# Optimization experiments

Hardware: AMD Instinct MI355X
Metric: run time of the kernel (lower is better)

## Reference

```python
import jax, jax.numpy as jnp
import numpy as np

N_NODES = 16384
K_NBR = 16
N_HOPS = 4  # hops + 2
IN_DIM = 256
RAW_DIM = 128
OUT_DIM = 64
PHI_DIM = 16
N_KERN = 4
E = N_NODES * K_NBR


def setup_inputs() -> dict:
    key = jax.random.key(0)
    ks = jax.random.split(key, 16)
    s = 0.05  # small weight scale for numerical sanity
    h = jax.random.normal(ks[0], (N_NODES, IN_DIM), jnp.float32)
    e_tensor = jax.random.normal(ks[1], (N_HOPS, N_NODES, RAW_DIM), jnp.float32)
    # kNN-style edges: each dst node has exactly K_NBR incoming edges
    src = jax.random.randint(ks[2], (N_HOPS, E), 0, N_NODES, jnp.int32)
    dst = jnp.tile(jnp.repeat(jnp.arange(N_NODES, dtype=jnp.int32), K_NBR)[None, :], (N_HOPS, 1))
    return {
        'h': h,
        'e_tensor': e_tensor,
        'src': src,
        'dst': dst,
        'W_phi': jax.random.normal(ks[3], (N_HOPS, RAW_DIM, PHI_DIM - 1), jnp.float32) * s,
        'mlp_w1': jax.random.normal(ks[4], (N_HOPS, RAW_DIM, IN_DIM), jnp.float32) * s,
        'mlp_b1': jax.random.normal(ks[5], (N_HOPS, IN_DIM), jnp.float32) * s,
        'mlp_w2': jax.random.normal(ks[6], (N_HOPS, IN_DIM, PHI_DIM * N_KERN), jnp.float32) * s,
        'mlp_b2': jax.random.normal(ks[7], (N_HOPS, PHI_DIM * N_KERN), jnp.float32) * s,
        'tilde_phi': jax.random.normal(ks[8], (N_HOPS, N_KERN, PHI_DIM), jnp.float32),
        'W': jax.random.normal(ks[9], (N_HOPS, IN_DIM, OUT_DIM * N_KERN), jnp.float32) * s,
        'bias': jax.random.normal(ks[10], (N_HOPS, OUT_DIM), jnp.float32) * s,
        'z': jax.random.normal(ks[11], (OUT_DIM, 1), jnp.float32),
    }


def _deform_gconv(h, e_l, src, dst, W_phi, w1, b1, w2, b2, tilde_phi, W, bias):
    N = h.shape[0]
    nk, phi_dim = tilde_phi.shape
    hk = (h @ W).reshape(N, nk, -1)                                  # (N, nk, out)
    phi = e_l @ W_phi                                                # (N, phi-1)
    tn = tilde_phi / jnp.linalg.norm(tilde_phi, axis=1, keepdims=True)  # (nk, phi)
    hid = jax.nn.relu(e_l @ w1 + b1)
    delta = (hid @ w2 + b2).reshape(N, nk, phi_dim)                  # (N, nk, phi)
    delta_ik = tn[None, :, :] + delta                                # (N, nk, phi)
    # per-edge quantities (edges carry dst-node delta_ik, u_sub_v distance)
    dist = phi[src] - phi[dst]                                       # (E, phi-1)
    last = jnp.all(dist == 0, axis=1, keepdims=True).astype(dist.dtype)
    dist = jnp.concatenate([dist, last], axis=1)                     # (E, phi)
    dist = dist / jnp.maximum(jnp.linalg.norm(dist, axis=1, keepdims=True), 1e-8)
    logits = jnp.einsum('ep,ekp->ek', dist, delta_ik[dst])           # (E, nk)
    # edge_softmax over incoming edges of each dst node
    mx = jax.ops.segment_max(logits, dst, num_segments=N)
    ex = jnp.exp(logits - mx[dst])
    den = jax.ops.segment_sum(ex, dst, num_segments=N)
    att = ex / den[dst]                                              # (E, nk)
    # message passing: m = h[src] * att, sum over incoming edges
    m = hk[src] * att[:, :, None]                                    # (E, nk, out)
    agg = jax.ops.segment_sum(m, dst, num_segments=N)                # (N, nk, out)
    out = agg.sum(1) + bias[None, :]
    out = out / jnp.maximum(jnp.linalg.norm(out, axis=1, keepdims=True), 1e-8)
    # regularizers
    d = tn[:, None, :] - tn[None, :, :]                              # (nk, nk, phi)
    l_sep = jnp.sum(jnp.sum(d * d, axis=-1)) / nk                    # sum_i mean_j ||t_i - t_j||^2
    l_focus = jnp.mean(jnp.sum(delta * delta, axis=2))
    return out, l_sep, l_focus


def reference(h, e_tensor, src, dst, W_phi, mlp_w1, mlp_b1, mlp_w2, mlp_b2, tilde_phi, W, bias, z):
    outs, l_seps, l_fos = jax.vmap(
        _deform_gconv, in_axes=(None, 0, 0, 0, 0, 0, 0, 0, 0, 0, 0, 0)
    )(h, e_tensor, src, dst, W_phi, mlp_w1, mlp_b1, mlp_w2, mlp_b2, tilde_phi, W, bias)
    # hop-level softmax fusion
    score = jnp.einsum('hno,oz->hnz', outs, z)                       # (n_hops, N, 1)
    att = jax.nn.softmax(score, axis=0)
    tilde_h = jnp.sum(att * outs, axis=0)                            # (N, out)
    l_sep = jnp.mean(l_seps)
    l_focus = jnp.mean(l_fos)
    return tilde_h, l_sep, l_focus
```

## Files before the change

kernel.cpp:

```cpp
#include <hip/hip_runtime.h>
#include <hip/hip_bf16.h>

#define N_NODES 16384
#define K_NBR 16
#define HOPS 4
#define IN_DIM 256
#define RAW_DIM 128
#define OUT_DIM 64
#define PHI_DIM 16
#define N_KERN 4
#define E_EDGES (N_NODES * K_NBR)

typedef __hip_bfloat16 bf16;
typedef __attribute__((ext_vector_type(8))) short short8;
typedef __attribute__((ext_vector_type(4))) float f32x4;
typedef __attribute__((ext_vector_type(2))) float f32x2;
typedef __attribute__((ext_vector_type(4))) unsigned int uint4v;

__device__ __forceinline__ float toF(float x) { return x; }
__device__ __forceinline__ float toF(bf16 x) { return __bfloat162float(x); }
__device__ __forceinline__ short f2bfbits(float f)
{
    bf16 b = __float2bfloat16(f);
    short s; __builtin_memcpy(&s, &b, 2); return s;
}

#define SWZ(row, colShort) ((colShort) ^ (((row) & 7) << 3))
#define SWZ32(row, colShort) ((colShort) ^ ((((row) >> 1) & 3) << 3))

__device__ __forceinline__ void gld_lds16(const bf16* g, short* l)
{
    __builtin_amdgcn_global_load_lds(
        (const __attribute__((address_space(1))) unsigned int*)g,
        (__attribute__((address_space(3))) unsigned int*)l, 16, 0, 0);
}

template <int IMM>
__device__ __forceinline__ float swzx(float v)
{
    return __builtin_bit_cast(float,
        __builtin_amdgcn_ds_swizzle(__builtin_bit_cast(int, v), IMM));
}
#define XOR1  0x041F
#define XOR2  0x081F
#define XOR4  0x101F
#define XOR8  0x201F
#define XOR16 0x401F

__device__ __forceinline__ void pkfma_w0(f32x2& acc, f32x2 w, f32x2 x)
{
    asm("v_pk_fma_f32 %0, %1, %2, %0 op_sel:[0,0,0] op_sel_hi:[0,1,1]"
        : "+v"(acc) : "v"(w), "v"(x));
}
__device__ __forceinline__ void pkfma_w1(f32x2& acc, f32x2 w, f32x2 x)
{
    asm("v_pk_fma_f32 %0, %1, %2, %0 op_sel:[1,0,0] op_sel_hi:[1,1,1]"
        : "+v"(acc) : "v"(w), "v"(x));
}

#define CV_WPHI 0
#define CV_W1   (CV_WPHI + HOPS * RAW_DIM * (PHI_DIM - 1))
#define CV_B1   (CV_W1 + HOPS * RAW_DIM * IN_DIM)
#define CV_W2   (CV_B1 + HOPS * IN_DIM)
#define CV_B2   (CV_W2 + HOPS * IN_DIM * PHI_DIM * N_KERN)
#define CV_TPHI (CV_B2 + HOPS * PHI_DIM * N_KERN)
#define CV_W    (CV_TPHI + HOPS * N_KERN * PHI_DIM)
#define CV_BIAS (CV_W + HOPS * IN_DIM * OUT_DIM * N_KERN)
#define CV_Z    (CV_BIAS + HOPS * OUT_DIM)
#define CV_END  (CV_Z + OUT_DIM)

#define WT_N  (HOPS * 256 * 256)
#define W1T_N (HOPS * 256 * 128)
#define W2T_N (HOPS * 64 * 256)
#define WPT_N (HOPS * 16 * 128)
#define CVT_TOTAL (WT_N + W1T_N + W2T_N + WPT_N)

#define NB_CV ((CV_END + 255) / 256)
#define NB_WT (CVT_TOTAL / 256)
#define NB_H  (N_NODES * 256 / 8 / 256)
#define NB_E  (HOPS * N_NODES * 128 / 8 / 256)
#define NB_ALL (NB_CV + NB_WT + NB_H + NB_E + 1)

#define GA_TOTAL 2048

__device__ __forceinline__ float loadDyn(const void* p, int i, bool isbf)
{
    return isbf ? toF(((const bf16*)p)[i]) : ((const float*)p)[i];
}

__device__ __forceinline__ void cvt8(bf16* dst, const void* src, size_t base, bool isbf)
{
    short8 v;
    if (isbf) {
        v = *(const short8*)((const bf16*)src + base);
    } else {
        const float* sp = (const float*)src + base;
        f32x4 f0 = *(const f32x4*)sp;
        f32x4 f1 = *(const f32x4*)(sp + 4);
#pragma unroll
        for (int j = 0; j < 4; j++) { v[j] = f2bfbits(f0[j]); v[4 + j] = f2bfbits(f1[j]); }
    }
    *(short8*)(dst + base) = v;
}

__global__ __launch_bounds__(256) void cvt_all(
    const void* h, const void* e,
    const void* wphi, const void* w1, const void* b1, const void* w2,
    const void* b2, const void* tphi, const void* W, const void* bias,
    const void* z, float* __restrict__ CV,
    bf16* __restrict__ wt, bf16* __restrict__ w1t, bf16* __restrict__ w2t,
    bf16* __restrict__ wpt, bf16* __restrict__ h_bf, bf16* __restrict__ e_bf,
    float* __restrict__ tn_out, float* __restrict__ acc, int* __restrict__ flagOut)
{
    __shared__ float s_det[4];
    int tid = threadIdx.x;
    {
        unsigned short pv = ((const unsigned short*)h)[tid];
        unsigned int bits = ((unsigned int)pv) << 16;
        float v; __builtin_memcpy(&v, &bits, 4);
        v = fabsf(v);
        if (!(v == v) || v > 1e30f) v = 1e30f;
#pragma unroll
        for (int off = 32; off > 0; off >>= 1) v = fmaxf(v, __shfl_xor(v, off));
        if ((tid & 63) == 0) s_det[tid >> 6] = v;
    }
    __syncthreads();
    bool isbf = fmaxf(fmaxf(s_det[0], s_det[1]), fmaxf(s_det[2], s_det[3])) < 1e4f;

    int b = blockIdx.x;
    if (b == NB_ALL - 1) {
        __shared__ float s_v[256], s_tn[256], s_red[256], s_hop[4];
        int hop = tid >> 6, t64 = tid & 63;
        int row = t64 >> 4, p = t64 & 15;
        float v = loadDyn(tphi, hop * 64 + t64, isbf);
        s_v[tid] = v;
        __syncthreads();
        float ss = 0.f;
        for (int q = 0; q < 16; q++) { float x = s_v[hop * 64 + row * 16 + q]; ss += x * x; }
        float tnv = v / sqrtf(ss);
        tn_out[hop * 64 + t64] = tnv;
        s_tn[tid] = tnv;
        __syncthreads();
        float s = 0.f;
        for (int j = 0; j < 4; j++) {
            float d = tnv - s_tn[hop * 64 + j * 16 + p];
            s += d * d;
        }
        s_red[tid] = s;
        __syncthreads();
        if (t64 == 0) {
            float tot = 0.f;
            for (int i = 0; i < 64; i++) tot += s_red[hop * 64 + i];
            s_hop[hop] = tot;
        }
        __syncthreads();
        if (tid == 0) {
            acc[0] = (s_hop[0] + s_hop[1] + s_hop[2] + s_hop[3]) * 0.0625f;
            acc[1] = 0.f;
            *flagOut = isbf ? 1 : 0;
        }
        return;
    }
    if (b < NB_CV) {
        int idx = b * 256 + tid;
        if (idx >= CV_END) return;
        float v;
        if      (idx < CV_W1)   v = loadDyn(wphi, idx - CV_WPHI, isbf);
        else if (idx < CV_B1)   v = loadDyn(w1,   idx - CV_W1,   isbf);
        else if (idx < CV_W2)   v = loadDyn(b1,   idx - CV_B1,   isbf);
        else if (idx < CV_B2)   v = loadDyn(w2,   idx - CV_W2,   isbf);
        else if (idx < CV_TPHI) v = loadDyn(b2,   idx - CV_B2,   isbf);
        else if (idx < CV_W)    v = loadDyn(tphi, idx - CV_TPHI, isbf);
        else if (idx < CV_BIAS) v = loadDyn(W,    idx - CV_W,    isbf);
        else if (idx < CV_Z)    v = loadDyn(bias, idx - CV_BIAS, isbf);
        else                    v = loadDyn(z,    idx - CV_Z,    isbf);
        CV[idx] = v;
        return;
    }
    b -= NB_CV;
    if (b < NB_WT) {
        int idx = b * 256 + tid;
        if (idx < WT_N) {
            int o = idx, hop = o >> 16, rem = o & 65535, n = rem >> 8, k = rem & 255;
            wt[o] = __float2bfloat16(loadDyn(W, hop * 65536 + k * 256 + n, isbf));
        } else if (idx < WT_N + W1T_N) {
            int o = idx - WT_N, hop = o >> 15, rem = o & 32767, n = rem >> 7, k = rem & 127;
            w1t[o] = __float2bfloat16(loadDyn(w1, hop * 32768 + k * 256 + n, isbf));
        } else if (idx < WT_N + W1T_N + W2T_N) {
            int o = idx - WT_N - W1T_N, hop = o >> 14, rem = o & 16383, n = rem >> 8, k = rem & 255;
            w2t[o] = __float2bfloat16(loadDyn(w2, hop * 16384 + k * 64 + n, isbf));
        } else {
            int o = idx - WT_N - W1T_N - W2T_N, hop = o >> 11, rem = o & 2047, n = rem >> 7, k = rem & 127;
            float v = (n < 15) ? loadDyn(wphi, hop * 1920 + k * 15 + n, isbf) : 0.f;
            wpt[o] = __float2bfloat16(v);
        }
        return;
    }
    b -= NB_WT;
    if (b < NB_H) {
        size_t base = ((size_t)b * 256 + tid) * 8;
        cvt8(h_bf, h, base, isbf);
        return;
    }
    b -= NB_H;
    {
        size_t base = ((size_t)b * 256 + tid) * 8;
        cvt8(e_bf, e, base, isbf);
    }
}

__device__ __forceinline__ void gemm_hk_dev(
    char* smem, const bf16* __restrict__ A, const bf16* __restrict__ Bt,
    unsigned char* __restrict__ Cg, int colBase, int rowBase)
{
    short* base = (short*)smem;
    int tid = threadIdx.x;
    int w = tid >> 6, lane = tid & 63;
    int wr = w >> 1, wc = w & 1;
    int l16 = lane & 15, quad = lane >> 4;
    f32x4 acc[4][4] = {};

#define HK_STAGE(bufb, k0v)                                                          \
    {                                                                                \
        short* As_ = base + (bufb) * 8192;                                           \
        short* Bs_ = As_ + 4096;                                                     \
        for (int id = tid; id < 128 * 4; id += 256) {                                \
            int row = id >> 2, j = id & 3;                                           \
            gld_lds16(A + (size_t)(rowBase + row) * 256 + (k0v) +                    \
                          ((j ^ ((row >> 1) & 3)) * 8),                              \
                      As_ + id * 8);                                                 \
        }                                                                            \
        for (int id = tid; id < 128 * 4; id += 256) {                                \
            int row = id >> 2, j = id & 3;                                           \
            gld_lds16(Bt + (size_t)(colBase + row) * 256 + (k0v) +                   \
                          ((j ^ ((row >> 1) & 3)) * 8),                              \
                      Bs_ + id * 8);                                                 \
        }                                                                            \
    }

    HK_STAGE(0, 0)
    __syncthreads();
    for (int t = 0; t < 8; ++t) {
        if (t < 7) HK_STAGE((t + 1) & 1, (t + 1) * 32)
        short* As = base + (t & 1) * 8192;
        short* Bs = As + 4096;
        short8 aF[4], bF[4];
#pragma unroll
        for (int mi = 0; mi < 4; mi++) {
            int row = wr * 64 + mi * 16 + l16;
            aF[mi] = *(const short8*)&As[row * 32 + SWZ32(row, quad * 8)];
        }
#pragma unroll
        for (int ni = 0; ni < 4; ni++) {
            int row = wc * 64 + ni * 16 + l16;
            bF[ni] = *(const short8*)&Bs[row * 32 + SWZ32(row, quad * 8)];
        }
#pragma unroll
        for (int mi = 0; mi < 4; mi++)
#pragma unroll
            for (int ni = 0; ni < 4; ni++)
                acc[mi][ni] = __builtin_amdgcn_mfma_f32_16x16x32_bf16(
                    aF[mi], bF[ni], acc[mi][ni], 0, 0, 0);
        __syncthreads();
    }
#undef HK_STAGE

    unsigned char* Cs = (unsigned char*)smem;
#pragma unroll
    for (int mi = 0; mi < 4; mi++)
#pragma unroll
        for (int ni = 0; ni < 4; ni++) {
            int cl = wc * 64 + ni * 16 + l16;
#pragma unroll
            for (int r = 0; r < 4; r++) {
                int rl = wr * 64 + mi * 16 + quad * 4 + r;
                float v = acc[mi][ni][r];
                int pk = __builtin_amdgcn_cvt_pk_fp8_f32(v, v, 0, false);
                Cs[rl * 128 + cl] = (unsigned char)(pk & 0xFF);
            }
        }
    __syncthreads();
    for (int c = tid; c < 128 * 8; c += 256) {
        int r = c >> 3, off = (c & 7) * 16;
        *(uint4v*)(Cg + ((size_t)(rowBase + r) * 256 + colBase) + off) =
            *(const uint4v*)(Cs + (size_t)r * 128 + off);
    }
}

__device__ __forceinline__ void hid_delta_dev(
    char* smem,
    const bf16* __restrict__ A, const bf16* __restrict__ B1,
    const bf16* __restrict__ B2, const bf16* __restrict__ WP,
    const float* __restrict__ b1, const float* __restrict__ b2,
    const float* __restrict__ tn, float* __restrict__ Dg,
    float* __restrict__ phiG, float* __restrict__ lfocus, int rowBase)
{
    short* As  = (short*)smem;
    short* Bs  = As + 64 * 64;
    short* Wpa = As + 20480;
    short* Hs  = (short*)smem;
    short* B2s = Hs + 64 * 256;
    float* Ds  = (float*)smem;
    float* s_w = (float*)(smem + 40944);

    int tid = threadIdx.x;
    int w = tid >> 6, lane = tid & 63;
    int l16 = lane & 15, quad = lane >> 4;

    {
        f32x4 acc[4][4] = {};
        f32x4 accp[4] = {};
        for (int k0 = 0; k0 < 128; k0 += 64) {
            for (int id = tid; id < 64 * 8; id += 256) {
                int row = id >> 3, j = id & 7;
                gld_lds16(A + (size_t)(rowBase + row) * 128 + k0 + ((j ^ (row & 7)) * 8),
                          As + id * 8);
            }
            for (int id = tid; id < 256 * 8; id += 256) {
                int row = id >> 3, j = id & 7;
                gld_lds16(B1 + (size_t)row * 128 + k0 + ((j ^ (row & 7)) * 8),
                          Bs + id * 8);
            }
            if (k0 == 0) {
                int row = tid >> 4, j = tid & 15;
                gld_lds16(WP + (size_t)row * 128 + ((j ^ (row & 7)) * 8),
                          Wpa + tid * 8);
            }
            __syncthreads();
#pragma unroll
            for (int kc = 0; kc < 64; kc += 32) {
                short8 aF[4], bF[4];
#pragma unroll
                for (int mi = 0; mi < 4; mi++) {
                    int row = mi * 16 + l16;
                    aF[mi] = *(const short8*)&As[row * 64 + SWZ(row, kc + quad * 8)];
                }
#pragma unroll
                for (int ni = 0; ni < 4; ni++) {
                    int row = w * 64 + ni * 16 + l16;
                    bF[ni] = *(const short8*)&Bs[row * 64 + SWZ(row, kc + quad * 8)];
                }
#pragma unroll
                for (int mi = 0; mi < 4; mi++)
#pragma unroll
                    for (int ni = 0; ni < 4; ni++)
                        acc[mi][ni] = __builtin_amdgcn_mfma_f32_16x16x32_bf16(
                            aF[mi], bF[ni], acc[mi][ni], 0, 0, 0);
                if (w == 0) {
                    short8 bFp = *(const short8*)&Wpa[l16 * 128 + SWZ(l16, k0 + kc + quad * 8)];
#pragma unroll
                    for (int mi = 0; mi < 4; mi++)
                        accp[mi] = __builtin_amdgcn_mfma_f32_16x16x32_bf16(
                            aF[mi], bFp, accp[mi], 0, 0, 0);
                }
            }
            __syncthreads();
        }
#pragma unroll
        for (int mi = 0; mi < 4; mi++) {
#pragma unroll
            for (int ni = 0; ni < 4; ni++) {
                int col = w * 64 + ni * 16 + l16;
                float bv = b1[col];
#pragma unroll
                for (int r = 0; r < 4; r++) {
                    int row = mi * 16 + quad * 4 + r;
                    float v = fmaxf(acc[mi][ni][r] + bv, 0.f);
                    Hs[row * 256 + SWZ(row, col)] = f2bfbits(v);
                }
            }
        }
        for (int id = tid; id < 64 * 8; id += 256) {
            int row = id >> 3, j = id & 7;
            gld_lds16(B2 + (size_t)row * 256 + ((j ^ (row & 7)) * 8),
                      B2s + id * 8);
        }
        if (w == 0) {
#pragma unroll
            for (int mi = 0; mi < 4; mi++)
#pragma unroll
                for (int r = 0; r < 4; r++)
                    phiG[(size_t)(rowBase + mi * 16 + quad * 4 + r) * 16 + l16] =
                        accp[mi][r];
        }
    }

    {
        f32x4 acc2[4] = {};
        for (int q = 0; q < 4; q++) {
            __syncthreads();
#pragma unroll
            for (int kcq = 0; kcq < 64; kcq += 32) {
                int arow = w * 16 + l16;
                short8 aF = *(const short8*)&Hs[arow * 256 + SWZ(arow, q * 64 + kcq + quad * 8)];
                short8 bF[4];
#pragma unroll
                for (int ni = 0; ni < 4; ni++) {
                    int row = ni * 16 + l16;
                    bF[ni] = *(const short8*)&B2s[row * 64 + SWZ(row, kcq + quad * 8)];
                }
#pragma unroll
                for (int ni = 0; ni < 4; ni++)
                    acc2[ni] = __builtin_amdgcn_mfma_f32_16x16x32_bf16(aF, bF[ni], acc2[ni], 0, 0, 0);
            }
            if (q < 3) {
                __syncthreads();
                for (int id = tid; id < 64 * 8; id += 256) {
                    int row = id >> 3, j = id & 7;
                    gld_lds16(B2 + (size_t)row * 256 + (q + 1) * 64 + ((j ^ (row & 7)) * 8),
                              B2s + id * 8);
                }
            }
        }
        __syncthreads();
        float sq = 0.f;
#pragma unroll
        for (int ni = 0; ni < 4; ni++) {
            int col = ni * 16 + l16;
            float bv = b2[col], tv = tn[col];
#pragma unroll
            for (int r = 0; r < 4; r++) {
                int row = w * 16 + quad * 4 + r;
                float v = acc2[ni][r] + bv;
                sq += v * v;
                Ds[row * 64 + col] = v + tv;
            }
        }
#pragma unroll
        for (int off = 32; off > 0; off >>= 1) sq += __shfl_xor(sq, off);
        if (lane == 0) s_w[w] = sq;
        __syncthreads();
        for (int c = tid; c < 64 * 16; c += 256) {
            int r = c >> 4, off = (c & 15) * 4;
            *(uint4v*)(Dg + (size_t)(rowBase + r) * 64 + off) =
                *(const uint4v*)(Ds + (size_t)r * 64 + off);
        }
        if (tid == 0) atomicAdd(lfocus, s_w[0] + s_w[1] + s_w[2] + s_w[3]);
    }
}

__global__ __launch_bounds__(256) void gemm_all(
    const bf16* __restrict__ h_bf, const bf16* __restrict__ e_bf,
    const bf16* __restrict__ WT, const bf16* __restrict__ WPT,
    const bf16* __restrict__ W1T, const bf16* __restrict__ W2T,
    const float* __restrict__ b1All, const float* __restrict__ b2All,
    const float* __restrict__ tnAll, unsigned char* __restrict__ hk_f8,
    float* __restrict__ phi, float* __restrict__ DELTA, float* __restrict__ lfocus)
{
    __shared__ __align__(16) char smem[45056];
    int b = blockIdx.x;
    bool isA = ((b >> 3) & 1) == 0;
    int a = ((b >> 4) << 3) | (b & 7);
    int hop = a >> 8;
    if (isA) {
        int r = a & 255, part = r >> 7, row = r & 127;
        gemm_hk_dev(smem, h_bf, WT + (size_t)hop * 65536,
                    hk_f8 + (size_t)hop * N_NODES * 256, part * 128, row * 128);
    } else {
        int tile = a & 255;
        hid_delta_dev(smem,
            e_bf + (size_t)hop * N_NODES * 128,
            W1T + (size_t)hop * 32768, W2T + (size_t)hop * 16384,
            WPT + (size_t)hop * 2048,
            b1All + hop * 256, b2All + hop * 64, tnAll + hop * 64,
            DELTA + (size_t)hop * N_NODES * 64,
            phi + (size_t)hop * N_NODES * 16, lfocus, tile * 64);
    }
}

__global__ __launch_bounds__(256) void edge_agg2(
    const unsigned char* __restrict__ hk, const float* __restrict__ phi,
    const float* __restrict__ dik, const int* __restrict__ src,
    const float* __restrict__ biasAll, float* __restrict__ outs)
{
    int b = blockIdx.x;
    int hop = b & 3;
    int wave = threadIdx.x >> 6, lane = threadIdx.x & 63;
    int node = (b >> 2) * 4 + wave;
    const unsigned char* hk_l = hk + (size_t)hop * N_NODES * 256;
    const float* phi_l  = phi + (size_t)hop * N_NODES * 16;
    const float* dik_l  = dik + (size_t)hop * N_NODES * 64;
    const int*   src_n  = src + (size_t)hop * E_EDGES + (size_t)node * 16;
    const float* bias_l = biasAll + hop * 64;
    float*       outs_n = outs + ((size_t)hop * N_NODES + node) * 64;

    __shared__ __align__(16) float s_dik[4][64];
    __shared__ __align__(16) float s_attT[4][4][24];
    __shared__ int   s_src[4][16];

    s_dik[wave][lane] = dik_l[(size_t)node * 64 + lane];
    if (lane < 16) s_src[wave][lane] = src_n[lane];

    int e = lane >> 2, q = lane & 3;
    int sN = s_src[wave][e];
    f32x4 ps = *(const f32x4*)(phi_l + (size_t)sN * 16 + q * 4);
    f32x4 pd = *(const f32x4*)(phi_l + (size_t)node * 16 + q * 4);
    float d0 = ps[0] - pd[0], d1 = ps[1] - pd[1];
    float d2 = ps[2] - pd[2], d3 = ps[3] - pd[3];
    bool q3 = (q == 3);
    float ssp = d0 * d0 + d1 * d1 + d2 * d2 + (q3 ? 0.f : d3 * d3);
    ssp += swzx<XOR1>(ssp); ssp += swzx<XOR2>(ssp);
    float last = (ssp == 0.f) ? 1.f : 0.f;
    if (q3) d3 = last;
    float inv = fminf(__builtin_amdgcn_rsqf(ssp + last * last), 1e8f);
#pragma unroll
    for (int k = 0; k < 4; k++) {
        f32x4 dkv = *(const f32x4*)&s_dik[wave][k * 16 + q * 4];
        float pk = d0 * dkv[0] + d1 * dkv[1] + d2 * dkv[2] + d3 * dkv[3];
        pk += swzx<XOR1>(pk); pk += swzx<XOR2>(pk);
        if (q == k) s_attT[wave][k][e] = pk * inv;
    }

    int k2 = lane & 3;
    float lgv = s_attT[wave][k2][e];
    float mx = lgv;
    mx = fmaxf(mx, swzx<XOR4>(mx));
    mx = fmaxf(mx, swzx<XOR8>(mx));
    mx = fmaxf(mx, swzx<XOR16>(mx));
    mx = fmaxf(mx, __shfl_xor(mx, 32));
    float ex = __expf(lgv - mx);
    float den = ex;
    den += swzx<XOR4>(den);
    den += swzx<XOR8>(den);
    den += swzx<XOR16>(den);
    den += __shfl_xor(den, 32);
    s_attT[wave][k2][e] = ex * __builtin_amdgcn_rcpf(den);

    int kk = lane >> 4, dsub = (lane & 15) * 4;
    f32x2 att2[8];
#pragma unroll
    for (int g = 0; g < 8; g++) att2[g] = *(const f32x2*)&s_attT[wave][kk][g * 2];
    f32x2 a01 = {0.f, 0.f}, a23 = {0.f, 0.f};
#pragma unroll
    for (int ep = 0; ep < 8; ep++) {
        int sm0 = __builtin_amdgcn_readfirstlane(s_src[wave][2 * ep]);
        int sm1 = __builtin_amdgcn_readfirstlane(s_src[wave][2 * ep + 1]);
        unsigned int u0 = *(const unsigned int*)(hk_l + (size_t)sm0 * 256 + lane * 4);
        unsigned int u1 = *(const unsigned int*)(hk_l + (size_t)sm1 * 256 + lane * 4);
        f32x2 w = att2[ep];
        pkfma_w0(a01, w, __builtin_amdgcn_cvt_pk_f32_fp8((int)u0, false));
        pkfma_w0(a23, w, __builtin_amdgcn_cvt_pk_f32_fp8((int)u0, true));
        pkfma_w1(a01, w, __builtin_amdgcn_cvt_pk_f32_fp8((int)u1, false));
        pkfma_w1(a23, w, __builtin_amdgcn_cvt_pk_f32_fp8((int)u1, true));
    }
    float a0 = a01[0], a1 = a01[1], a2 = a23[0], a3 = a23[1];
    a0 += swzx<XOR16>(a0); a0 += __shfl_xor(a0, 32);
    a1 += swzx<XOR16>(a1); a1 += __shfl_xor(a1, 32);
    a2 += swzx<XOR16>(a2); a2 += __shfl_xor(a2, 32);
    a3 += swzx<XOR16>(a3); a3 += __shfl_xor(a3, 32);
    f32x4 bv = *(const f32x4*)(bias_l + dsub);
    float o0 = a0 + bv[0];
    float o1 = a1 + bv[1];
    float o2 = a2 + bv[2];
    float o3 = a3 + bv[3];
    float ssq = o0 * o0 + o1 * o1 + o2 * o2 + o3 * o3;
    ssq += swzx<XOR1>(ssq);
    ssq += swzx<XOR2>(ssq);
    ssq += swzx<XOR4>(ssq);
    ssq += swzx<XOR8>(ssq);
    float inv2 = fminf(__builtin_amdgcn_rsqf(ssq), 1e8f);
    if (kk == 0) {
        f32x4 st;
        st[0] = o0 * inv2; st[1] = o1 * inv2; st[2] = o2 * inv2; st[3] = o3 * inv2;
        *(f32x4*)(outs_n + dsub) = st;
    }
}

__global__ __launch_bounds__(256) void fuse_kernel(
    const float* __restrict__ outs, const float* __restrict__ z,
    void* __restrict__ out, const int* __restrict__ flag,
    const float* __restrict__ acc)
{
    int tid = threadIdx.x;
    int node = blockIdx.x * 4 + (tid >> 6);
    int dd = tid & 63;
    float zv = z[dd];
    float o[4], sc[4];
#pragma unroll
    for (int h = 0; h < 4; h++) {
        o[h] = outs[((size_t)h * N_NODES + node) * 64 + dd];
        float v = o[h] * zv;
#pragma unroll
        for (int off = 32; off > 0; off >>= 1) v += __shfl_xor(v, off);
        sc[h] = v;
    }
    float mx = fmaxf(fmaxf(sc[0], sc[1]), fmaxf(sc[2], sc[3]));
    float e0 = __expf(sc[0] - mx), e1 = __expf(sc[1] - mx);
    float e2 = __expf(sc[2] - mx), e3 = __expf(sc[3] - mx);
    float den = e0 + e1 + e2 + e3;
    float t = (e0 * o[0] + e1 * o[1] + e2 * o[2] + e3 * o[3]) * __builtin_amdgcn_rcpf(den);
    size_t oi = (size_t)node * 64 + dd;
    bool isbf = (*flag != 0);
    if (isbf) ((bf16*)out)[oi] = __float2bfloat16(t);
    else      ((float*)out)[oi] = t;
    if (blockIdx.x == 0 && tid == 0) {
        float a = acc[0];
        float b = acc[1] / ((float)N_NODES * 4.f * 4.f);
        size_t base = (size_t)N_NODES * 64;
        if (isbf) {
            ((bf16*)out)[base]     = __float2bfloat16(a);
            ((bf16*)out)[base + 1] = __float2bfloat16(b);
        } else {
            ((float*)out)[base]     = a;
            ((float*)out)[base + 1] = b;
        }
    }
}

extern "C" void kernel_launch(void* const* d_in, const int* in_sizes, int n_in,
                              void* d_out, int out_size, void* d_ws, size_t ws_size,
                              hipStream_t stream)
{
    const void* h    = d_in[0];
    const void* e    = d_in[1];
    const int*  src  = (const int*)d_in[2];
    const void* Wphi = d_in[4];
    const void* w1   = d_in[5];
    const void* b1   = d_in[6];
    const void* w2   = d_in[7];
    const void* b2   = d_in[8];
    const void* tphi = d_in[9];
    const void* W    = d_in[10];
    const void* bias = d_in[11];
    const void* z    = d_in[12];

    float* ws    = (float*)d_ws;
    float* CV    = ws;
    float* OUTS  = CV + CV_END;
    float* PHI   = OUTS + (size_t)4 * N_NODES * 64;
    float* DELTA = PHI + (size_t)4 * N_NODES * 16;
    float* TN    = DELTA + (size_t)4 * N_NODES * 64;
    float* ACC   = TN + 256;
    int*   FLAG  = (int*)(ACC + 2);
    bf16*  H_BF  = (bf16*)(ACC + 4);
    bf16*  E_BF  = H_BF + (size_t)N_NODES * 256;
    bf16*  WT    = E_BF + (size_t)HOPS * N_NODES * 128;
    bf16*  W1T   = WT + WT_N;
    bf16*  W2T   = W1T + W1T_N;
    bf16*  WPT   = W2T + W2T_N;
    unsigned char* HK_F8 = (unsigned char*)(WPT + WPT_N);

    cvt_all<<<NB_ALL, 256, 0, stream>>>(
        h, e, Wphi, w1, b1, w2, b2, tphi, W, bias, z, CV,
        WT, W1T, W2T, WPT, H_BF, E_BF, TN, ACC, FLAG);

    gemm_all<<<dim3(GA_TOTAL), 256, 0, stream>>>(
        H_BF, E_BF, WT, WPT, W1T, W2T,
        CV + CV_B1, CV + CV_B2, TN, HK_F8, PHI, DELTA, ACC + 1);

    edge_agg2<<<dim3(N_NODES), 256, 0, stream>>>(
        HK_F8, PHI, DELTA, src, CV + CV_BIAS, OUTS);

    fuse_kernel<<<dim3(N_NODES / 4), 256, 0, stream>>>(
        OUTS, CV + CV_Z, d_out, FLAG, ACC);
}
```

Measured before the change: 200.5 us.

## Compact constant copy, coarsen conversion blocks, remap GEMM block order

The constant buffer now holds only the biases and z vector, no longer the full weight matrices, which the GEMMs read from transposed bf16 copies anyway. The conversion kernel processes more elements per thread (4 weight elements, 8 vector chunks), cutting block count. The GEMM block index mapping is reordered so that the eight blocks sharing a row-group span hop and column halves, which is meant to improve L2 reuse of the h rows across concurrently running blocks.

```diff
diff --git a/kernel.cpp b/kernel.cpp
--- a/kernel.cpp
+++ b/kernel.cpp
@@ -58,16 +58,11 @@
         : "+v"(acc) : "v"(w), "v"(x));
 }
 
-#define CV_WPHI 0
-#define CV_W1   (CV_WPHI + HOPS * RAW_DIM * (PHI_DIM - 1))
-#define CV_B1   (CV_W1 + HOPS * RAW_DIM * IN_DIM)
-#define CV_W2   (CV_B1 + HOPS * IN_DIM)
-#define CV_B2   (CV_W2 + HOPS * IN_DIM * PHI_DIM * N_KERN)
-#define CV_TPHI (CV_B2 + HOPS * PHI_DIM * N_KERN)
-#define CV_W    (CV_TPHI + HOPS * N_KERN * PHI_DIM)
-#define CV_BIAS (CV_W + HOPS * IN_DIM * OUT_DIM * N_KERN)
-#define CV_Z    (CV_BIAS + HOPS * OUT_DIM)
-#define CV_END  (CV_Z + OUT_DIM)
+#define CVC_B1   0
+#define CVC_B2   (CVC_B1 + HOPS * IN_DIM)
+#define CVC_BIAS (CVC_B2 + HOPS * PHI_DIM * N_KERN)
+#define CVC_Z    (CVC_BIAS + HOPS * OUT_DIM)
+#define CVC_END  (CVC_Z + OUT_DIM)
 
 #define WT_N  (HOPS * 256 * 256)
 #define W1T_N (HOPS * 256 * 128)
@@ -75,10 +70,10 @@
 #define WPT_N (HOPS * 16 * 128)
 #define CVT_TOTAL (WT_N + W1T_N + W2T_N + WPT_N)
 
-#define NB_CV ((CV_END + 255) / 256)
-#define NB_WT (CVT_TOTAL / 256)
-#define NB_H  (N_NODES * 256 / 8 / 256)
-#define NB_E  (HOPS * N_NODES * 128 / 8 / 256)
+#define NB_CV ((CVC_END + 255) / 256)
+#define NB_WT (CVT_TOTAL / 1024)
+#define NB_H  (N_NODES * 256 / 8 / 2048)
+#define NB_E  (HOPS * N_NODES * 128 / 8 / 2048)
 #define NB_ALL (NB_CV + NB_WT + NB_H + NB_E + 1)
 
 #define GA_TOTAL 2048
@@ -163,49 +158,54 @@
     }
     if (b < NB_CV) {
         int idx = b * 256 + tid;
-        if (idx >= CV_END) return;
+        if (idx >= CVC_END) return;
         float v;
-        if      (idx < CV_W1)   v = loadDyn(wphi, idx - CV_WPHI, isbf);
-        else if (idx < CV_B1)   v = loadDyn(w1,   idx - CV_W1,   isbf);
-        else if (idx < CV_W2)   v = loadDyn(b1,   idx - CV_B1,   isbf);
-        else if (idx < CV_B2)   v = loadDyn(w2,   idx - CV_W2,   isbf);
-        else if (idx < CV_TPHI) v = loadDyn(b2,   idx - CV_B2,   isbf);
-        else if (idx < CV_W)    v = loadDyn(tphi, idx - CV_TPHI, isbf);
-        else if (idx < CV_BIAS) v = loadDyn(W,    idx - CV_W,    isbf);
-        else if (idx < CV_Z)    v = loadDyn(bias, idx - CV_BIAS, isbf);
-        else                    v = loadDyn(z,    idx - CV_Z,    isbf);
+        if      (idx < CVC_B2)   v = loadDyn(b1,   idx - CVC_B1,   isbf);
+        else if (idx < CVC_BIAS) v = loadDyn(b2,   idx - CVC_B2,   isbf);
+        else if (idx < CVC_Z)    v = loadDyn(bias, idx - CVC_BIAS, isbf);
+        else                     v = loadDyn(z,    idx - CVC_Z,    isbf);
         CV[idx] = v;
         return;
     }
     b -= NB_CV;
     if (b < NB_WT) {
-        int idx = b * 256 + tid;
-        if (idx < WT_N) {
-            int o = idx, hop = o >> 16, rem = o & 65535, n = rem >> 8, k = rem & 255;
-            wt[o] = __float2bfloat16(loadDyn(W, hop * 65536 + k * 256 + n, isbf));
-        } else if (idx < WT_N + W1T_N) {
-            int o = idx - WT_N, hop = o >> 15, rem = o & 32767, n = rem >> 7, k = rem & 127;
-            w1t[o] = __float2bfloat16(loadDyn(w1, hop * 32768 + k * 256 + n, isbf));
-        } else if (idx < WT_N + W1T_N + W2T_N) {
-            int o = idx - WT_N - W1T_N, hop = o >> 14, rem = o & 16383, n = rem >> 8, k = rem & 255;
-            w2t[o] = __float2bfloat16(loadDyn(w2, hop * 16384 + k * 64 + n, isbf));
-        } else {
-            int o = idx - WT_N - W1T_N - W2T_N, hop = o >> 11, rem = o & 2047, n = rem >> 7, k = rem & 127;
-            float v = (n < 15) ? loadDyn(wphi, hop * 1920 + k * 15 + n, isbf) : 0.f;
-            wpt[o] = __float2bfloat16(v);
+        int base = (b * 256 + tid) * 4;
+#pragma unroll
+        for (int jj = 0; jj < 4; jj++) {
+            int idx = base + jj;
+            if (idx < WT_N) {
+                int o = idx, hop = o >> 16, rem = o & 65535, n = rem >> 8, k = rem & 255;
+                wt[o] = __float2bfloat16(loadDyn(W, hop * 65536 + k * 256 + n, isbf));
+            } else if (idx < WT_N + W1T_N) {
+                int o = idx - WT_N, hop = o >> 15, rem = o & 32767, n = rem >> 7, k = rem & 127;
+                w1t[o] = __float2bfloat16(loadDyn(w1, hop * 32768 + k * 256 + n, isbf));
+            } else if (idx < WT_N + W1T_N + W2T_N) {
+                int o = idx - WT_N - W1T_N, hop = o >> 14, rem = o & 16383, n = rem >> 8, k = rem & 255;
+                w2t[o] = __float2bfloat16(loadDyn(w2, hop * 16384 + k * 64 + n, isbf));
+            } else {
+                int o = idx - WT_N - W1T_N - W2T_N, hop = o >> 11, rem = o & 2047, n = rem >> 7, k = rem & 127;
+                float v = (n < 15) ? loadDyn(wphi, hop * 1920 + k * 15 + n, isbf) : 0.f;
+                wpt[o] = __float2bfloat16(v);
+            }
         }
         return;
     }
     b -= NB_WT;
     if (b < NB_H) {
-        size_t base = ((size_t)b * 256 + tid) * 8;
-        cvt8(h_bf, h, base, isbf);
+#pragma unroll
+        for (int k = 0; k < 8; k++) {
+            size_t base = ((size_t)b * 2048 + k * 256 + tid) * 8;
+            cvt8(h_bf, h, base, isbf);
+        }
         return;
     }
     b -= NB_H;
     {
-        size_t base = ((size_t)b * 256 + tid) * 8;
-        cvt8(e_bf, e, base, isbf);
+#pragma unroll
+        for (int k = 0; k < 8; k++) {
+            size_t base = ((size_t)b * 2048 + k * 256 + tid) * 8;
+            cvt8(e_bf, e, base, isbf);
+        }
     }
 }
 
@@ -449,15 +449,18 @@
 {
     __shared__ __align__(16) char smem[45056];
     int b = blockIdx.x;
-    bool isA = ((b >> 3) & 1) == 0;
-    int a = ((b >> 4) << 3) | (b & 7);
-    int hop = a >> 8;
-    if (isA) {
-        int r = a & 255, part = r >> 7, row = r & 127;
+    int x = b & 7;
+    int p = b >> 3;
+    int s = p >> 1;
+    if ((p & 1) == 0) {
+        int rg = x * 16 + (s >> 3);
+        int v = s & 7;
+        int hop = v >> 1, part = v & 1;
         gemm_hk_dev(smem, h_bf, WT + (size_t)hop * 65536,
-                    hk_f8 + (size_t)hop * N_NODES * 256, part * 128, row * 128);
+                    hk_f8 + (size_t)hop * N_NODES * 256, part * 128, rg * 128);
     } else {
-        int tile = a & 255;
+        int hop = x & 3;
+        int tile = ((x >> 2) << 7) + s;
         hid_delta_dev(smem,
             e_bf + (size_t)hop * N_NODES * 128,
             W1T + (size_t)hop * 32768, W2T + (size_t)hop * 16384,
@@ -626,7 +629,7 @@
 
     float* ws    = (float*)d_ws;
     float* CV    = ws;
-    float* OUTS  = CV + CV_END;
+    float* OUTS  = CV + CVC_END;
     float* PHI   = OUTS + (size_t)4 * N_NODES * 64;
     float* DELTA = PHI + (size_t)4 * N_NODES * 16;
     float* TN    = DELTA + (size_t)4 * N_NODES * 64;
@@ -646,11 +649,11 @@
 
     gemm_all<<<dim3(GA_TOTAL), 256, 0, stream>>>(
         H_BF, E_BF, WT, WPT, W1T, W2T,
-        CV + CV_B1, CV + CV_B2, TN, HK_F8, PHI, DELTA, ACC + 1);
+        CV + CVC_B1, CV + CVC_B2, TN, HK_F8, PHI, DELTA, ACC + 1);
 
     edge_agg2<<<dim3(N_NODES), 256, 0, stream>>>(
-        HK_F8, PHI, DELTA, src, CV + CV_BIAS, OUTS);
+        HK_F8, PHI, DELTA, src, CV + CVC_BIAS, OUTS);
 
     fuse_kernel<<<dim3(N_NODES / 4), 256, 0, stream>>>(
-        OUTS, CV + CV_Z, d_out, FLAG, ACC);
-}
+        OUTS, CV + CVC_Z, d_out, FLAG, ACC);
+}
```

After: 194.8 us. 1.03x faster.
